# Performance work log

Hardware: AMD Instinct MI355X
Metric: run time of the kernel (lower is better)

## Reference

```python
import jax, jax.numpy as jnp
import numpy as np

EPS = 1e-5
V = 16  # num_nodes

def _bn(x, g, b, axes, ch):
    # training-mode BatchNorm (biased variance), channel axis = ch
    m = x.mean(axes, keepdims=True)
    v = x.var(axes, keepdims=True)
    sh = [1] * x.ndim
    sh[ch] = x.shape[ch]
    return (x - m) * jax.lax.rsqrt(v + EPS) * g.reshape(sh) + b.reshape(sh)

def _adp(nv1, nv2, max_num_neigh=1):
    # softmax(relu(nv1 @ nv2), dim=1), then keep entries > max(1/V, (k+1)-th largest) with straight-through mask
    A = jax.nn.softmax(jax.nn.relu(nv1 @ nv2), axis=1)
    kth = -jnp.sort(-A, axis=1)[:, max_num_neigh:max_num_neigh + 1]  # (k+1)-th largest per row == -kthvalue(-A, k+1)
    mask = ((A > 1.0 / A.shape[0]) & (A > kth)).astype(A.dtype)
    binm = jax.lax.stop_gradient(mask - A) + A  # straight-through estimator
    return A * binm

def _stgcn(x, A, gw, gb, b1g, b1b, tw, tb, b2g, b2b):
    # standard ST-GCN block with spatial kernel K=1, stride 1, identity residual (in==out)
    # x: (N,C,T,V)
    res = x
    y = jnp.einsum('oc,nctv->notv', gw, x) + gb[None, :, None, None]  # 1x1 conv
    y = jnp.einsum('nctv,vw->nctw', y, A)                              # graph aggregation
    y = jax.nn.relu(_bn(y, b1g, b1b, (0, 2, 3), 1))
    y = jax.lax.conv_general_dilated(y, tw[:, :, :, None], (1, 1), [(1, 1), (0, 0)],
                                     dimension_numbers=('NCHW', 'OIHW', 'NCHW'))  # temporal conv (kt,1)
    y = _bn(y + tb[None, :, None, None], b2g, b2b, (0, 2, 3), 1)
    return jax.nn.relu(y + res)

def _static(x, pw, pg, pb, tw, tg, tb):
    # x: (p,n,c,s)
    p, n, c, s = x.shape
    # p-branch: Conv1d(c->c, k=1, no bias) over node dim + BN1d (stats over n*s batch and length p)
    y = jnp.einsum('oc,pncs->nsop', pw, x)          # (n,s,c,p)
    y = _bn(y, pg, pb, (0, 1, 3), 2)
    # t-branch: grouped Conv1d over time, groups = p nodes, kernel 3, pad 1
    z = y.transpose(0, 3, 2, 1).reshape(n, p * c, s)
    z = jax.lax.conv_general_dilated(z, tw, (1,), [(1, 1)],
                                     dimension_numbers=('NCH', 'OIH', 'NCH'),
                                     feature_group_count=p)
    z = _bn(z, tg, tb, (0, 2), 1)
    return z.reshape(n, p, c, s).transpose(1, 0, 2, 3)  # (p,n,c,s)

def _forward(x, nv1, nv2,
             d1gw, d1gb, d1b1g, d1b1b, d1tw, d1tb, d1b2g, d1b2b,
             d2gw, d2gb, d2b1g, d2b1b, d2tw, d2tb, d2b2g, d2b2b,
             s1pw, s1pg, s1pb, s1tw, s1tg, s1tb,
             s2pw, s2pg, s2pb, s2tw, s2tg, s2tb):
    A = _adp(nv1, nv2, 1)
    d = _stgcn(x, A, d1gw, d1gb, d1b1g, d1b1b, d1tw, d1tb, d1b2g, d1b2b)
    d = _stgcn(d, A, d2gw, d2gb, d2b1g, d2b1b, d2tw, d2tb, d2b2g, d2b2b)
    d = d.max(axis=2)                      # (N,C,V) max over time
    xs = x.transpose(3, 0, 1, 2)           # (V,N,C,T)
    s = _static(xs, s1pw, s1pg, s1pb, s1tw, s1tg, s1tb)
    s = _static(s, s2pw, s2pg, s2pb, s2tw, s2tg, s2tb)
    s = s.transpose(1, 2, 3, 0).max(axis=2)  # (N,C,V)
    return jnp.concatenate([d, s], axis=2)   # (N,C,2V)

def setup_inputs():
    key = jax.random.key(0)
    N, C, T, kt = 32, 128, 256, 3
    ks = jax.random.split(key, 8)
    def nrm(k, sh, s=0.05):
        return jax.random.normal(k, sh, jnp.float32) * s
    inp = {'x': nrm(ks[0], (N, C, T, V), 1.0),
           'nv1': nrm(ks[1], (V, 64), 1.0),
           'nv2': nrm(ks[2], (64, V), 1.0)}
    def stgcn_p(k, pre):
        k1, k2 = jax.random.split(k)
        return {pre + 'gw': nrm(k1, (C, C)), pre + 'gb': jnp.zeros(C),
                pre + 'b1g': jnp.ones(C), pre + 'b1b': jnp.zeros(C),
                pre + 'tw': nrm(k2, (C, C, kt)), pre + 'tb': jnp.zeros(C),
                pre + 'b2g': jnp.ones(C), pre + 'b2b': jnp.zeros(C)}
    def static_p(k, pre):
        k1, k2 = jax.random.split(k)
        return {pre + 'pw': nrm(k1, (C, C)), pre + 'pg': jnp.ones(C), pre + 'pb': jnp.zeros(C),
                pre + 'tw': nrm(k2, (V * C, C, kt)), pre + 'tg': jnp.ones(V * C), pre + 'tb': jnp.zeros(V * C)}
    inp.update(stgcn_p(ks[3], 'd1'))
    inp.update(stgcn_p(ks[4], 'd2'))
    inp.update(static_p(ks[5], 's1'))
    inp.update(static_p(ks[6], 's2'))
    return inp

def reference(x, nv1, nv2,
              d1gw, d1gb, d1b1g, d1b1b, d1tw, d1tb, d1b2g, d1b2b,
              d2gw, d2gb, d2b1g, d2b1b, d2tw, d2tb, d2b2g, d2b2b,
              s1pw, s1pg, s1pb, s1tw, s1tg, s1tb,
              s2pw, s2pg, s2pb, s2tw, s2tg, s2tb):
    return _forward(x, nv1, nv2,
                    d1gw, d1gb, d1b1g, d1b1b, d1tw, d1tb, d1b2g, d1b2b,
                    d2gw, d2gb, d2b1g, d2b1b, d2tw, d2tb, d2b2g, d2b2b,
                    s1pw, s1pg, s1pb, s1tw, s1tg, s1tb,
                    s2pw, s2pg, s2pb, s2tw, s2tg, s2tb)
```

## Files before the change

### kernel.cpp

```cpp
#include <hip/hip_runtime.h>

#define EPSBN 1e-5f

typedef __attribute__((ext_vector_type(8))) __bf16 bf16x8;
typedef __attribute__((ext_vector_type(4))) float f32x4;
typedef __attribute__((ext_vector_type(8))) unsigned short us8;

__device__ inline unsigned short f2bf(float f) {
  __bf16 h = (__bf16)f;
  return __builtin_bit_cast(unsigned short, h);
}
__device__ inline float bf2f(unsigned short u) {
  __bf16 h = __builtin_bit_cast(__bf16, u);
  return (float)h;
}

__global__ void k_adj(const float* __restrict__ nv1, const float* __restrict__ nv2,
                      float* __restrict__ A, float* __restrict__ sA,
                      int* __restrict__ cntA, int* __restrict__ lvA, float* __restrict__ lvalA) {
  __shared__ float M[16][16];
  int tid = threadIdx.x;
  int i = tid >> 4, j = tid & 15;
  float acc = 0.f;
  #pragma unroll
  for (int k = 0; k < 64; ++k) acc += nv1[i*64+k] * nv2[k*16+j];
  M[i][j] = fmaxf(acc, 0.f);
  __syncthreads();
  if (tid < 16) {
    float m = -1e30f;
    for (int c = 0; c < 16; ++c) m = fmaxf(m, M[tid][c]);
    float e[16]; float s = 0.f;
    for (int c = 0; c < 16; ++c) { e[c] = expf(M[tid][c] - m); s += e[c]; }
    float inv = 1.f / s;
    float t1 = -1e30f, t2 = -1e30f;
    for (int c = 0; c < 16; ++c) {
      float a = e[c] * inv; e[c] = a;
      if (a > t1) { t2 = t1; t1 = a; }
      else if (a > t2) t2 = a;
    }
    for (int c = 0; c < 16; ++c) {
      bool keep = (e[c] > (1.0f/16.0f)) && (e[c] > t2);
      M[tid][c] = keep ? e[c] : 0.f;
    }
  }
  __syncthreads();
  A[tid] = M[tid>>4][tid&15];
  if (tid < 16) {
    float s = 0.f;
    int cnt = 0;
    for (int v = 0; v < 16; ++v) {
      float a = M[v][tid];
      s += a;
      if (a != 0.f) { lvA[tid*16 + cnt] = v; lvalA[tid*16 + cnt] = a; ++cnt; }
    }
    sA[tid] = s;
    cntA[tid] = cnt;
  }
}

__device__ inline void cvt_cw_seg(const float* w, unsigned short* o, int lidx) {
  o[lidx] = f2bf(w[lidx]);
}
__device__ inline void cvt_tw_seg(const float* w, unsigned short* o, int lidx) {
  int oo = lidx / 384;
  int r = lidx - oo*384;
  int tap = r >> 7, c = r & 127;
  o[lidx] = f2bf(w[(oo*128 + c)*3 + tap]);
}
__global__ __launch_bounds__(256) void k_cvt_dyn(
    const float* __restrict__ d1g, const float* __restrict__ d1t,
    const float* __restrict__ d2g, const float* __restrict__ d2t,
    unsigned short* __restrict__ O) {
  int b = blockIdx.x, tid = threadIdx.x;
  if (b < 64)        cvt_cw_seg(d1g, O,          b*256 + tid);
  else if (b < 256)  cvt_tw_seg(d1t, O + 16384, (b-64)*256 + tid);
  else if (b < 320)  cvt_cw_seg(d2g, O + 65536, (b-256)*256 + tid);
  else               cvt_tw_seg(d2t, O + 81920, (b-320)*256 + tid);
}
__global__ __launch_bounds__(256) void k_cvt_stat(
    const float* __restrict__ s1p, const float* __restrict__ s1t,
    const float* __restrict__ s2p, const float* __restrict__ s2t,
    unsigned short* __restrict__ S) {
  int b = blockIdx.x, tid = threadIdx.x;
  if (b < 64)        cvt_cw_seg(s1p, S,           b*256 + tid);
  else if (b < 3136) cvt_tw_seg(s1t, S + 16384,  (b-64)*256 + tid);
  else if (b < 3200) cvt_cw_seg(s2p, S + 802816, (b-3136)*256 + tid);
  else               cvt_tw_seg(s2t, S + 819200, (b-3200)*256 + tid);
}

__global__ __launch_bounds__(256) void k_xcvt(const float* __restrict__ x,
                                              unsigned short* __restrict__ xB,
                                              unsigned short* __restrict__ xS) {
  __shared__ float tl[64*128];
  int b = blockIdx.x; int n = b >> 6; int t0q = b & 63;
  int tid = threadIdx.x;
  const float* xb = x + (long)n*524288 + t0q*64;
  for (int idx = tid; idx < 2048; idx += 256) {
    int c = idx >> 4, q = idx & 15;
    float4 v = *(const float4*)(xb + (long)c*4096 + q*4);
    int cb = c >> 2, cl = c & 3;
    #pragma unroll
    for (int j = 0; j < 4; ++j)
      tl[(4*q+j)*128 + (((cb ^ q) & 31) << 2) + cl] = ((const float*)&v)[j];
  }
  __syncthreads();
  for (int idx = tid; idx < 1024; idx += 256) {
    int pos = idx >> 4, c8 = (idx & 15) << 3;
    int cb0 = c8 >> 2, cb1 = cb0 + 1, qp = pos >> 2;
    f32x4 v0 = *(const f32x4*)&tl[pos*128 + (((cb0 ^ qp) & 31) << 2)];
    f32x4 v1 = *(const f32x4*)&tl[pos*128 + (((cb1 ^ qp) & 31) << 2)];
    us8 pk;
    pk[0]=f2bf(v0.x); pk[1]=f2bf(v0.y); pk[2]=f2bf(v0.z); pk[3]=f2bf(v0.w);
    pk[4]=f2bf(v1.x); pk[5]=f2bf(v1.y); pk[6]=f2bf(v1.z); pk[7]=f2bf(v1.w);
    *(us8*)(xB + ((long)n*4096 + t0q*64 + pos)*128 + c8) = pk;
    int vv = pos & 15, tt = pos >> 4;
    *(us8*)(xS + ((long)(n*16+vv)*256 + t0q*4 + tt)*128 + c8) = pk;
  }
}

__global__ __launch_bounds__(256) void k_aggGconv(
    const unsigned short* __restrict__ xB,
    const int* __restrict__ cntA, const int* __restrict__ lvA, const float* __restrict__ lvalA,
    const unsigned short* __restrict__ Wb,
    unsigned short* __restrict__ out,
    const float* __restrict__ gb, const float* __restrict__ sAv,
    float* __restrict__ part)
{
  __shared__ __align__(16) unsigned short Th[64*128];
  __shared__ int cntS[16];
  __shared__ int lvS[256];
  __shared__ float lvalS[256];
  int b = blockIdx.x; int n = b >> 6; int off = (b & 63) << 6;
  int tid = threadIdx.x;
  if (tid < 16) cntS[tid] = cntA[tid];
  lvS[tid] = lvA[tid];
  lvalS[tid] = lvalA[tid];
  __syncthreads();
  const unsigned short* xbase = xB + ((long)n*4096 + off)*128;
  for (int idx = tid; idx < 1024; idx += 256) {
    int pos = idx >> 4, c8 = (idx & 15) << 3;
    int tt = pos >> 4, w = pos & 15;
    float s[8];
    #pragma unroll
    for (int k = 0; k < 8; ++k) s[k] = 0.f;
    int cw = cntS[w];
    for (int j = 0; j < cw; ++j) {
      int p = tt*16 + lvS[w*16 + j];
      float a = lvalS[w*16 + j];
      us8 raw = *(const us8*)(xbase + (long)p*128 + c8);
      #pragma unroll
      for (int k = 0; k < 8; ++k) s[k] += a * bf2f(raw[k]);
    }
    us8 pk;
    #pragma unroll
    for (int k = 0; k < 8; ++k) pk[k] = f2bf(s[k]);
    int byteoff = (pos << 8) + (c8 << 1);
    byteoff ^= ((pos & 7) << 4);
    *(us8*)((char*)Th + byteoff) = pk;
  }
  __syncthreads();
  int wv = tid >> 6, lane = tid & 63, l15 = lane & 15, lhi = lane >> 4;
  int o0 = wv << 5;
  f32x4 zz = {0.f,0.f,0.f,0.f};
  f32x4 acc[2][4];
  #pragma unroll
  for (int i = 0; i < 2; ++i)
    #pragma unroll
    for (int q = 0; q < 4; ++q) acc[i][q] = zz;
  const unsigned short* wr0 = Wb + (long)(o0 + l15)*128 + lhi*8;
  const unsigned short* wr1 = wr0 + 16*128;
  #pragma unroll
  for (int kk = 0; kk < 4; ++kk) {
    int kc = kk*32 + lhi*8;
    bf16x8 a0 = *(const bf16x8*)(wr0 + kk*32);
    bf16x8 a1 = *(const bf16x8*)(wr1 + kk*32);
    #pragma unroll
    for (int pf = 0; pf < 4; ++pf) {
      int row = pf*16 + l15;
      int byteoff = (row << 8) + (kc << 1);
      byteoff ^= ((row & 7) << 4);
      bf16x8 bh = *(const bf16x8*)((const char*)Th + byteoff);
      acc[0][pf] = __builtin_amdgcn_mfma_f32_16x16x32_bf16(a0, bh, acc[0][pf], 0, 0, 0);
      acc[1][pf] = __builtin_amdgcn_mfma_f32_16x16x32_bf16(a1, bh, acc[1][pf], 0, 0, 0);
    }
  }
  float s1a[2][4], s2a[2][4];
  #pragma unroll
  for (int i = 0; i < 2; ++i)
    #pragma unroll
    for (int j = 0; j < 4; ++j) { s1a[i][j] = 0.f; s2a[i][j] = 0.f; }
  unsigned short* og = out + ((long)n*4096 + off)*128;
  #pragma unroll
  for (int of = 0; of < 2; ++of) {
    int oc = o0 + of*16 + lhi*4;
    #pragma unroll
    for (int pf = 0; pf < 4; ++pf) {
      int pos = pf*16 + l15;
      f32x4 r = acc[of][pf];
      float s = sAv[l15];
      r.x += gb[oc+0]*s; r.y += gb[oc+1]*s;
      r.z += gb[oc+2]*s; r.w += gb[oc+3]*s;
      ushort4 pk;
      pk.x = f2bf(r.x); pk.y = f2bf(r.y); pk.z = f2bf(r.z); pk.w = f2bf(r.w);
      *(ushort4*)(og + (long)pos*128 + oc) = pk;
      #pragma unroll
      for (int j = 0; j < 4; ++j) { s1a[of][j] += r[j]; s2a[of][j] += r[j]*r[j]; }
    }
  }
  #pragma unroll
  for (int of = 0; of < 2; ++of)
    #pragma unroll
    for (int j = 0; j < 4; ++j) {
      float a = s1a[of][j], b2 = s2a[of][j];
      #pragma unroll
      for (int m = 1; m < 16; m <<= 1) { a += __shfl_xor(a, m); b2 += __shfl_xor(b2, m); }
      s1a[of][j] = a; s2a[of][j] = b2;
    }
  if (l15 == 0) {
    #pragma unroll
    for (int of = 0; of < 2; ++of) {
      int ch = o0 + of*16 + lhi*4;
      f32x4 w1 = {s1a[of][0], s1a[of][1], s1a[of][2], s1a[of][3]};
      f32x4 w2 = {s2a[of][0], s2a[of][1], s2a[of][2], s2a[of][3]};
      *(f32x4*)&part[(long)blockIdx.x*256 + ch] = w1;
      *(f32x4*)&part[(long)blockIdx.x*256 + 128 + ch] = w2;
    }
  }
}

__global__ __launch_bounds__(256) void k_combineAggGconv(
    const unsigned short* __restrict__ z, const unsigned short* __restrict__ xB,
    const int* __restrict__ cntA, const int* __restrict__ lvA, const float* __restrict__ lvalA,
    const float* __restrict__ sc, const float* __restrict__ sh,
    const unsigned short* __restrict__ Wb,
    unsigned short* __restrict__ r2, unsigned short* __restrict__ out,
    const float* __restrict__ gb, const float* __restrict__ sAv,
    float* __restrict__ part)
{
  __shared__ __align__(16) unsigned short rl[64*128];
  __shared__ __align__(16) unsigned short Th[64*128];
  __shared__ int cntS[16];
  __shared__ int lvS[256];
  __shared__ float lvalS[256];
  int b = blockIdx.x;
  int tid = threadIdx.x;
  if (tid < 16) cntS[tid] = cntA[tid];
  lvS[tid] = lvA[tid];
  lvalS[tid] = lvalA[tid];
  long zbase = (long)b * 8192;
  for (int idx = tid; idx < 1024; idx += 256) {
    int pos = idx >> 4, c8 = (idx & 15) << 3;
    us8 zr = *(const us8*)(z  + zbase + (long)pos*128 + c8);
    us8 xr = *(const us8*)(xB + zbase + (long)pos*128 + c8);
    us8 pr;
    #pragma unroll
    for (int k = 0; k < 8; ++k) {
      int cc = c8 + k;
      float v = bf2f(zr[k]) * sc[cc] + sh[cc] + bf2f(xr[k]);
      pr[k] = f2bf(fmaxf(v, 0.f));
    }
    *(us8*)(rl + pos*128 + c8) = pr;
    *(us8*)(r2 + zbase + (long)pos*128 + c8) = pr;
  }
  __syncthreads();
  for (int idx = tid; idx < 1024; idx += 256) {
    int pos = idx >> 4, c8 = (idx & 15) << 3;
    int tt = pos >> 4, w = pos & 15;
    float s[8];
    #pragma unroll
    for (int k = 0; k < 8; ++k) s[k] = 0.f;
    int cw = cntS[w];
    for (int j = 0; j < cw; ++j) {
      int p = tt*16 + lvS[w*16 + j];
      float a = lvalS[w*16 + j];
      us8 raw = *(const us8*)(rl + p*128 + c8);
      #pragma unroll
      for (int k = 0; k < 8; ++k) s[k] += a * bf2f(raw[k]);
    }
    us8 pk;
    #pragma unroll
    for (int k = 0; k < 8; ++k) pk[k] = f2bf(s[k]);
    int byteoff = (pos << 8) + (c8 << 1);
    byteoff ^= ((pos & 7) << 4);
    *(us8*)((char*)Th + byteoff) = pk;
  }
  __syncthreads();
  int wv = tid >> 6, lane = tid & 63, l15 = lane & 15, lhi = lane >> 4;
  int o0 = wv << 5;
  f32x4 zz = {0.f,0.f,0.f,0.f};
  f32x4 acc[2][4];
  #pragma unroll
  for (int i = 0; i < 2; ++i)
    #pragma unroll
    for (int q = 0; q < 4; ++q) acc[i][q] = zz;
  const unsigned short* wr0 = Wb + (long)(o0 + l15)*128 + lhi*8;
  const unsigned short* wr1 = wr0 + 16*128;
  #pragma unroll
  for (int kk = 0; kk < 4; ++kk) {
    int kc = kk*32 + lhi*8;
    bf16x8 a0 = *(const bf16x8*)(wr0 + kk*32);
    bf16x8 a1 = *(const bf16x8*)(wr1 + kk*32);
    #pragma unroll
    for (int pf = 0; pf < 4; ++pf) {
      int row = pf*16 + l15;
      int byteoff = (row << 8) + (kc << 1);
      byteoff ^= ((row & 7) << 4);
      bf16x8 bh = *(const bf16x8*)((const char*)Th + byteoff);
      acc[0][pf] = __builtin_amdgcn_mfma_f32_16x16x32_bf16(a0, bh, acc[0][pf], 0, 0, 0);
      acc[1][pf] = __builtin_amdgcn_mfma_f32_16x16x32_bf16(a1, bh, acc[1][pf], 0, 0, 0);
    }
  }
  float s1a[2][4], s2a[2][4];
  #pragma unroll
  for (int i = 0; i < 2; ++i)
    #pragma unroll
    for (int j = 0; j < 4; ++j) { s1a[i][j] = 0.f; s2a[i][j] = 0.f; }
  unsigned short* og = out + zbase;
  #pragma unroll
  for (int of = 0; of < 2; ++of) {
    int oc = o0 + of*16 + lhi*4;
    #pragma unroll
    for (int pf = 0; pf < 4; ++pf) {
      int pos = pf*16 + l15;
      f32x4 r = acc[of][pf];
      float s = sAv[l15];
      r.x += gb[oc+0]*s; r.y += gb[oc+1]*s;
      r.z += gb[oc+2]*s; r.w += gb[oc+3]*s;
      ushort4 pk;
      pk.x = f2bf(r.x); pk.y = f2bf(r.y); pk.z = f2bf(r.z); pk.w = f2bf(r.w);
      *(ushort4*)(og + (long)pos*128 + oc) = pk;
      #pragma unroll
      for (int j = 0; j < 4; ++j) { s1a[of][j] += r[j]; s2a[of][j] += r[j]*r[j]; }
    }
  }
  #pragma unroll
  for (int of = 0; of < 2; ++of)
    #pragma unroll
    for (int j = 0; j < 4; ++j) {
      float a = s1a[of][j], b2 = s2a[of][j];
      #pragma unroll
      for (int m = 1; m < 16; m <<= 1) { a += __shfl_xor(a, m); b2 += __shfl_xor(b2, m); }
      s1a[of][j] = a; s2a[of][j] = b2;
    }
  if (l15 == 0) {
    #pragma unroll
    for (int of = 0; of < 2; ++of) {
      int ch = o0 + of*16 + lhi*4;
      f32x4 w1 = {s1a[of][0], s1a[of][1], s1a[of][2], s1a[of][3]};
      f32x4 w2 = {s2a[of][0], s2a[of][1], s2a[of][2], s2a[of][3]};
      *(f32x4*)&part[(long)blockIdx.x*256 + ch] = w1;
      *(f32x4*)&part[(long)blockIdx.x*256 + 128 + ch] = w2;
    }
  }
}

template<int POSB, int HALO, int TAPS, int GROUPED_W, int IN_BN, int GROUPED_BN, int RELU_IN>
__global__ __launch_bounds__(256) void k_conv(
    const unsigned short* __restrict__ in, const unsigned short* __restrict__ Wb,
    unsigned short* __restrict__ out, int L,
    const float* __restrict__ isc, const float* __restrict__ ish,
    float* __restrict__ part)
{
  constexpr int TW = POSB + 2*HALO;
  constexpr int PF = POSB / 16;
  constexpr int KT = TAPS*128;
  __shared__ __align__(16) unsigned short Th[TW*128];
  int tid = threadIdx.x;
  int bpg = L / POSB;
  int g = blockIdx.x / bpg;
  int pos0 = (blockIdx.x - g*bpg) * POSB;
  const unsigned short* ing = in + (long)g*L*128;

  int cbase = (IN_BN && GROUPED_BN) ? ((g & 15) << 7) : 0;
  for (int idx = tid; idx < TW*16; idx += 256) {
    int row = idx >> 4;
    int c8 = (idx & 15) << 3;
    int gp = pos0 + row - HALO;
    us8 h = (us8)0;
    if (gp >= 0 && gp < L) {
      us8 raw = *(const us8*)(ing + (long)gp*128 + c8);
      if (IN_BN) {
        #pragma unroll
        for (int j = 0; j < 8; ++j) {
          int ci = cbase + c8 + j;
          float v = bf2f(raw[j]) * isc[ci] + ish[ci];
          if (RELU_IN) v = fmaxf(v, 0.f);
          h[j] = f2bf(v);
        }
      } else {
        h = raw;
      }
    }
    int byteoff = (row << 8) + (c8 << 1);
    byteoff ^= ((row & 7) << 4);
    *(us8*)((char*)Th + byteoff) = h;
  }
  __syncthreads();

  int wv = tid >> 6, lane = tid & 63, l15 = lane & 15, lhi = lane >> 4;
  int o0 = wv << 5;

  f32x4 zz = {0.f,0.f,0.f,0.f};
  f32x4 acc[2][PF];
  #pragma unroll
  for (int i = 0; i < 2; ++i)
    #pragma unroll
    for (int q = 0; q < PF; ++q) acc[i][q] = zz;

  const unsigned short* Wg = Wb + (GROUPED_W ? (long)(g & 15)*128*KT : 0);
  const unsigned short* wr0 = Wg + (long)(o0 + l15)*KT + lhi*8;
  const unsigned short* wr1 = wr0 + 16*KT;

  #pragma unroll
  for (int tap = 0; tap < TAPS; ++tap) {
    #pragma unroll
    for (int kk = 0; kk < 4; ++kk) {
      int kc = kk*32 + lhi*8;
      bf16x8 a0 = *(const bf16x8*)(wr0 + tap*128 + kk*32);
      bf16x8 a1 = *(const bf16x8*)(wr1 + tap*128 + kk*32);
      #pragma unroll
      for (int pf = 0; pf < PF; ++pf) {
        int row = pf*16 + l15 + tap*HALO;
        int byteoff = (row << 8) + (kc << 1);
        byteoff ^= ((row & 7) << 4);
        bf16x8 bh = *(const bf16x8*)((const char*)Th + byteoff);
        acc[0][pf] = __builtin_amdgcn_mfma_f32_16x16x32_bf16(a0, bh, acc[0][pf], 0, 0, 0);
        acc[1][pf] = __builtin_amdgcn_mfma_f32_16x16x32_bf16(a1, bh, acc[1][pf], 0, 0, 0);
      }
    }
  }

  float s1a[2][4], s2a[2][4];
  #pragma unroll
  for (int i = 0; i < 2; ++i)
    #pragma unroll
    for (int j = 0; j < 4; ++j) { s1a[i][j] = 0.f; s2a[i][j] = 0.f; }
  #pragma unroll
  for (int of = 0; of < 2; ++of)
    #pragma unroll
    for (int pf = 0; pf < PF; ++pf) {
      f32x4 r = acc[of][pf];
      #pragma unroll
      for (int j = 0; j < 4; ++j) { s1a[of][j] += r[j]; s2a[of][j] += r[j]*r[j]; }
    }
  #pragma unroll
  for (int of = 0; of < 2; ++of)
    #pragma unroll
    for (int j = 0; j < 4; ++j) {
      float a = s1a[of][j], b2 = s2a[of][j];
      #pragma unroll
      for (int m = 1; m < 16; m <<= 1) { a += __shfl_xor(a, m); b2 += __shfl_xor(b2, m); }
      s1a[of][j] = a; s2a[of][j] = b2;
    }
  if (l15 == 0) {
    #pragma unroll
    for (int of = 0; of < 2; ++of) {
      int ch = o0 + of*16 + lhi*4;
      f32x4 w1 = {s1a[of][0], s1a[of][1], s1a[of][2], s1a[of][3]};
      f32x4 w2 = {s2a[of][0], s2a[of][1], s2a[of][2], s2a[of][3]};
      *(f32x4*)&part[(long)blockIdx.x*256 + ch] = w1;
      *(f32x4*)&part[(long)blockIdx.x*256 + 128 + ch] = w2;
    }
  }

  __syncthreads();
  #pragma unroll
  for (int of = 0; of < 2; ++of) {
    int oc = o0 + of*16 + lhi*4;
    #pragma unroll
    for (int pf = 0; pf < PF; ++pf) {
      int pos = pf*16 + l15;
      f32x4 r = acc[of][pf];
      ushort4 pk;
      pk.x = f2bf(r.x); pk.y = f2bf(r.y); pk.z = f2bf(r.z); pk.w = f2bf(r.w);
      int byteoff = (pos << 8) + (oc << 1);
      byteoff ^= ((pos & 7) << 4);
      *(ushort4*)((char*)Th + byteoff) = pk;
    }
  }
  __syncthreads();
  unsigned short* og = out + ((long)g*L + pos0)*128;
  for (int idx = tid; idx < POSB*16; idx += 256) {
    int row = idx >> 4, c8 = (idx & 15) << 3;
    int byteoff = (row << 8) + (c8 << 1);
    byteoff ^= ((row & 7) << 4);
    us8 v = *(const us8*)((const char*)Th + byteoff);
    *(us8*)(og + (long)row*128 + c8) = v;
  }
}

__global__ __launch_bounds__(256) void k_bnfin128(const float* __restrict__ part,
                           const float* __restrict__ gamma, const float* __restrict__ beta,
                           float* __restrict__ sc, float* __restrict__ sh,
                           float invN, int nblk) {
  int c = blockIdx.x, tid = threadIdx.x;
  float s1 = 0.f, s2 = 0.f;
  for (int b = tid; b < nblk; b += 256) {
    s1 += part[b*256 + c];
    s2 += part[b*256 + 128 + c];
  }
  __shared__ float l1[256], l2[256];
  l1[tid] = s1; l2[tid] = s2;
  __syncthreads();
  for (int st = 128; st > 0; st >>= 1) {
    if (tid < st) { l1[tid] += l1[tid+st]; l2[tid] += l2[tid+st]; }
    __syncthreads();
  }
  if (tid == 0) {
    float mean = l1[0]*invN;
    float var  = l2[0]*invN - mean*mean;
    float s = gamma[c] * rsqrtf(var + EPSBN);
    sc[c] = s;
    sh[c] = beta[c] - mean*s;
  }
}

__global__ void k_bnfin2048(const float* __restrict__ part,
                            const float* __restrict__ gamma, const float* __restrict__ beta,
                            float* __restrict__ sc, float* __restrict__ sh, float invN) {
  int ch = blockIdx.x; int v = ch >> 7, c = ch & 127;
  int lane = threadIdx.x;
  int n = lane >> 1, bp = lane & 1;
  int blk = ((n*16 + v) << 1) + bp;
  float s1 = part[blk*256 + c];
  float s2 = part[blk*256 + 128 + c];
  for (int m = 32; m > 0; m >>= 1) { s1 += __shfl_down(s1, m); s2 += __shfl_down(s2, m); }
  if (lane == 0) {
    float mean = s1*invN;
    float var  = s2*invN - mean*mean;
    float s = gamma[ch] * rsqrtf(var + EPSBN);
    sc[ch] = s;
    sh[ch] = beta[ch] - mean*s;
  }
}

__global__ __launch_bounds__(256) void k_maxdyn(
    const unsigned short* __restrict__ z, const unsigned short* __restrict__ res,
    const float* __restrict__ sc, const float* __restrict__ sh,
    float* __restrict__ outp)
{
  int b = blockIdx.x; int n = b >> 4, v = b & 15;
  int tid = threadIdx.x; int c = tid & 127, h = tid >> 7;
  const unsigned short* zb = z   + ((long)n*4096 + v)*128 + c;
  const unsigned short* rb = res + ((long)n*4096 + v)*128 + c;
  float s = sc[c], bb = sh[c];
  float m = 0.f;
  for (int t = h; t < 256; t += 2) {
    float val = bf2f(zb[(long)t*2048]) * s + bb + bf2f(rb[(long)t*2048]);
    m = fmaxf(m, val);
  }
  __shared__ float red[256];
  red[tid] = m;
  __syncthreads();
  if (tid < 128)
    outp[(long)n*4096 + c*32 + v] = fmaxf(fmaxf(red[tid], red[tid+128]), 0.f);
}

__global__ __launch_bounds__(256) void k_maxstat(
    const unsigned short* __restrict__ z,
    const float* __restrict__ sc, const float* __restrict__ sh,
    float* __restrict__ outp)
{
  int b = blockIdx.x; int n = b >> 4, v = b & 15;
  int tid = threadIdx.x; int c = tid & 127, h = tid >> 7;
  const unsigned short* zb = z + (long)b*256*128 + c;
  float s = sc[v*128 + c], bb = sh[v*128 + c];
  float m = -1e30f;
  for (int t = h; t < 256; t += 2)
    m = fmaxf(m, bf2f(zb[t*128]) * s + bb);
  __shared__ float red[256];
  red[tid] = m;
  __syncthreads();
  if (tid < 128)
    outp[(long)n*4096 + c*32 + 16 + v] = fmaxf(red[tid], red[tid+128]);
}

extern "C" void kernel_launch(void* const* d_in, const int* in_sizes, int n_in,
                              void* d_out, int out_size, void* d_ws, size_t ws_size,
                              hipStream_t stream) {
  (void)in_sizes; (void)n_in; (void)out_size; (void)ws_size;
  const float* x     = (const float*)d_in[0];
  const float* nv1   = (const float*)d_in[1];
  const float* nv2   = (const float*)d_in[2];
  const float* d1gw  = (const float*)d_in[3];
  const float* d1gb  = (const float*)d_in[4];
  const float* d1b1g = (const float*)d_in[5];
  const float* d1b1b = (const float*)d_in[6];
  const float* d1tw  = (const float*)d_in[7];
  const float* d1b2g = (const float*)d_in[9];
  const float* d1b2b = (const float*)d_in[10];
  const float* d2gw  = (const float*)d_in[11];
  const float* d2gb  = (const float*)d_in[12];
  const float* d2b1g = (const float*)d_in[13];
  const float* d2b1b = (const float*)d_in[14];
  const float* d2tw  = (const float*)d_in[15];
  const float* d2b2g = (const float*)d_in[17];
  const float* d2b2b = (const float*)d_in[18];
  const float* s1pw  = (const float*)d_in[19];
  const float* s1pg  = (const float*)d_in[20];
  const float* s1pb  = (const float*)d_in[21];
  const float* s1tw  = (const float*)d_in[22];
  const float* s1tg  = (const float*)d_in[23];
  const float* s1tb  = (const float*)d_in[24];
  const float* s2pw  = (const float*)d_in[25];
  const float* s2pg  = (const float*)d_in[26];
  const float* s2pb  = (const float*)d_in[27];
  const float* s2tw  = (const float*)d_in[28];
  const float* s2tg  = (const float*)d_in[29];
  const float* s2tb  = (const float*)d_in[30];

  float* W = (float*)d_ws;
  float* Am  = W;
  float* sAv = W + 256;
  float* scA = W + 512;  float* shA = W + 640;
  float* scB = W + 768;  float* shB = W + 896;
  float* scC = W + 1024; float* shC = W + 1152;
  float* scD = W + 1280; float* shD = W + 1408;
  float* scE = W + 1536; float* shE = W + 1664;
  float* scG = W + 1792; float* shG = W + 1920;
  float* scF = W + 2048; float* shF = W + 4096;
  float* scH = W + 6144; float* shH = W + 8192;
  int*   cntA  = (int*)(W + 10240);
  int*   lvA   = (int*)(W + 10496);
  float* lvalA = W + 10752;
  float* A = W + 16384;
  float* B = A + 16777216;
  float* C = B + 16777216;
  float* part = C + 16777216;
  float* outp = (float*)d_out;

  unsigned short* A0 = (unsigned short*)A;
  unsigned short* A1 = (unsigned short*)(A + 8388608);
  unsigned short* B0 = (unsigned short*)B;
  unsigned short* B1 = (unsigned short*)(B + 8388608);
  unsigned short* C0 = (unsigned short*)C;
  unsigned short* C1 = (unsigned short*)(C + 8388608);

  unsigned short* OW = (unsigned short*)d_out;
  unsigned short* w_d1g = OW;
  unsigned short* w_d1t = OW + 16384;
  unsigned short* w_d2g = OW + 65536;
  unsigned short* w_d2t = OW + 81920;
  unsigned short* SW    = B1;
  unsigned short* w_s1p = SW;
  unsigned short* w_s1t = SW + 16384;
  unsigned short* w_s2p = SW + 802816;
  unsigned short* w_s2t = SW + 819200;

  k_adj<<<1, 256, 0, stream>>>(nv1, nv2, Am, sAv, cntA, lvA, lvalA);
  k_cvt_dyn<<<512, 256, 0, stream>>>(d1gw, d1tw, d2gw, d2tw, OW);
  k_xcvt<<<2048, 256, 0, stream>>>(x, A0, A1);

  k_aggGconv<<<2048, 256, 0, stream>>>(A0, cntA, lvA, lvalA, w_d1g, B0, d1gb, sAv, part);
  k_bnfin128<<<128, 256, 0, stream>>>(part, d1b1g, d1b1b, scA, shA, 1.f/131072.f, 2048);
  k_conv<128,16,3,0,1,0,1><<<1024, 256, 0, stream>>>(B0, w_d1t, C0, 4096, scA, shA, part);
  k_bnfin128<<<128, 256, 0, stream>>>(part, d1b2g, d1b2b, scB, shB, 1.f/131072.f, 1024);
  k_combineAggGconv<<<2048, 256, 0, stream>>>(C0, A0, cntA, lvA, lvalA, scB, shB, w_d2g,
                                              B0, C1, d2gb, sAv, part);
  k_bnfin128<<<128, 256, 0, stream>>>(part, d2b1g, d2b1b, scC, shC, 1.f/131072.f, 2048);
  k_conv<128,16,3,0,1,0,1><<<1024, 256, 0, stream>>>(C1, w_d2t, B1, 4096, scC, shC, part);
  k_bnfin128<<<128, 256, 0, stream>>>(part, d2b2g, d2b2b, scD, shD, 1.f/131072.f, 1024);
  k_maxdyn<<<512, 256, 0, stream>>>(B1, B0, scD, shD, outp);

  k_cvt_stat<<<6272, 256, 0, stream>>>(s1pw, s1tw, s2pw, s2tw, SW);
  k_conv<128,0,1,0,0,0,0><<<1024, 256, 0, stream>>>(A1, w_s1p, C0, 256, nullptr, nullptr, part);
  k_bnfin128<<<128, 256, 0, stream>>>(part, s1pg, s1pb, scE, shE, 1.f/131072.f, 1024);
  k_conv<128,1,3,1,1,0,0><<<1024, 256, 0, stream>>>(C0, w_s1t, A0, 256, scE, shE, part);
  k_bnfin2048<<<2048, 64, 0, stream>>>(part, s1tg, s1tb, scF, shF, 1.f/8192.f);
  k_conv<128,0,1,0,1,1,0><<<1024, 256, 0, stream>>>(A0, w_s2p, C0, 256, scF, shF, part);
  k_bnfin128<<<128, 256, 0, stream>>>(part, s2pg, s2pb, scG, shG, 1.f/131072.f, 1024);
  k_conv<128,1,3,1,1,0,0><<<1024, 256, 0, stream>>>(C0, w_s2t, A0, 256, scG, shG, part);
  k_bnfin2048<<<2048, 64, 0, stream>>>(part, s2tg, s2tb, scH, shH, 1.f/8192.f);
  k_maxstat<<<512, 256, 0, stream>>>(A0, scH, shH, outp);
}
```

Baseline: 354.3 us.

## Fuse BN stat finalization into producer kernels via atomics and last-block reduction

New measurement: 1.174 ms. 231% more time.

```diff
diff --git a/kernel.cpp b/kernel.cpp
--- a/kernel.cpp
+++ b/kernel.cpp
@@ -15,11 +15,67 @@
   return (float)h;
 }
 
-__global__ void k_adj(const float* __restrict__ nv1, const float* __restrict__ nv2,
-                      float* __restrict__ A, float* __restrict__ sA,
-                      int* __restrict__ cntA, int* __restrict__ lvA, float* __restrict__ lvalA) {
+__device__ inline void bn_finalize_tail(float* acc, int* cnt, int nblk, int NCH,
+    const float* __restrict__ gamma, const float* __restrict__ beta,
+    float* __restrict__ sc, float* __restrict__ sh, float invN, int tid) {
+  __syncthreads();
+  __shared__ int lastFlag;
+  if (tid == 0) {
+    __threadfence();
+    lastFlag = (atomicAdd(cnt, 1) == nblk - 1) ? 1 : 0;
+  }
+  __syncthreads();
+  if (lastFlag) {
+    __threadfence();
+    for (int ch = tid; ch < NCH; ch += 256) {
+      float s1 = __hip_atomic_load(acc + ch,        __ATOMIC_RELAXED, __HIP_MEMORY_SCOPE_AGENT);
+      float s2 = __hip_atomic_load(acc + NCH + ch,  __ATOMIC_RELAXED, __HIP_MEMORY_SCOPE_AGENT);
+      float mean = s1 * invN;
+      float var  = s2 * invN - mean * mean;
+      float s = gamma[ch] * rsqrtf(var + EPSBN);
+      sc[ch] = s;
+      sh[ch] = beta[ch] - mean * s;
+    }
+  }
+}
+
+__device__ inline void cvt_cw_seg(const float* w, unsigned short* o, int lidx) {
+  o[lidx] = f2bf(w[lidx]);
+}
+__device__ inline void cvt_tw_seg(const float* w, unsigned short* o, int lidx) {
+  int oo = lidx / 384;
+  int r = lidx - oo*384;
+  int tap = r >> 7, c = r & 127;
+  o[lidx] = f2bf(w[(oo*128 + c)*3 + tap]);
+}
+__global__ __launch_bounds__(256) void k_setup(
+    const float* __restrict__ nv1, const float* __restrict__ nv2,
+    float* __restrict__ A, float* __restrict__ sA,
+    int* __restrict__ cntA, int* __restrict__ lvA, float* __restrict__ lvalA,
+    const float* __restrict__ d1g, const float* __restrict__ d1t,
+    const float* __restrict__ d2g, const float* __restrict__ d2t,
+    unsigned short* __restrict__ O,
+    const float* __restrict__ s1p, const float* __restrict__ s1t,
+    const float* __restrict__ s2p, const float* __restrict__ s2t,
+    unsigned short* __restrict__ S)
+{
+  int b = blockIdx.x, tid = threadIdx.x;
+  if (b < 512) {
+    if (b < 64)        cvt_cw_seg(d1g, O,          b*256 + tid);
+    else if (b < 256)  cvt_tw_seg(d1t, O + 16384, (b-64)*256 + tid);
+    else if (b < 320)  cvt_cw_seg(d2g, O + 65536, (b-256)*256 + tid);
+    else               cvt_tw_seg(d2t, O + 81920, (b-320)*256 + tid);
+    return;
+  }
+  if (b < 6784) {
+    int sb = b - 512;
+    if (sb < 64)        cvt_cw_seg(s1p, S,           sb*256 + tid);
+    else if (sb < 3136) cvt_tw_seg(s1t, S + 16384,  (sb-64)*256 + tid);
+    else if (sb < 3200) cvt_cw_seg(s2p, S + 802816, (sb-3136)*256 + tid);
+    else                cvt_tw_seg(s2t, S + 819200, (sb-3200)*256 + tid);
+    return;
+  }
   __shared__ float M[16][16];
-  int tid = threadIdx.x;
   int i = tid >> 4, j = tid & 15;
   float acc = 0.f;
   #pragma unroll
@@ -58,36 +114,6 @@
   }
 }
 
-__device__ inline void cvt_cw_seg(const float* w, unsigned short* o, int lidx) {
-  o[lidx] = f2bf(w[lidx]);
-}
-__device__ inline void cvt_tw_seg(const float* w, unsigned short* o, int lidx) {
-  int oo = lidx / 384;
-  int r = lidx - oo*384;
-  int tap = r >> 7, c = r & 127;
-  o[lidx] = f2bf(w[(oo*128 + c)*3 + tap]);
-}
-__global__ __launch_bounds__(256) void k_cvt_dyn(
-    const float* __restrict__ d1g, const float* __restrict__ d1t,
-    const float* __restrict__ d2g, const float* __restrict__ d2t,
-    unsigned short* __restrict__ O) {
-  int b = blockIdx.x, tid = threadIdx.x;
-  if (b < 64)        cvt_cw_seg(d1g, O,          b*256 + tid);
-  else if (b < 256)  cvt_tw_seg(d1t, O + 16384, (b-64)*256 + tid);
-  else if (b < 320)  cvt_cw_seg(d2g, O + 65536, (b-256)*256 + tid);
-  else               cvt_tw_seg(d2t, O + 81920, (b-320)*256 + tid);
-}
-__global__ __launch_bounds__(256) void k_cvt_stat(
-    const float* __restrict__ s1p, const float* __restrict__ s1t,
-    const float* __restrict__ s2p, const float* __restrict__ s2t,
-    unsigned short* __restrict__ S) {
-  int b = blockIdx.x, tid = threadIdx.x;
-  if (b < 64)        cvt_cw_seg(s1p, S,           b*256 + tid);
-  else if (b < 3136) cvt_tw_seg(s1t, S + 16384,  (b-64)*256 + tid);
-  else if (b < 3200) cvt_cw_seg(s2p, S + 802816, (b-3136)*256 + tid);
-  else               cvt_tw_seg(s2t, S + 819200, (b-3200)*256 + tid);
-}
-
 __global__ __launch_bounds__(256) void k_xcvt(const float* __restrict__ x,
                                               unsigned short* __restrict__ xB,
                                               unsigned short* __restrict__ xS) {
@@ -124,7 +150,9 @@
     const unsigned short* __restrict__ Wb,
     unsigned short* __restrict__ out,
     const float* __restrict__ gb, const float* __restrict__ sAv,
-    float* __restrict__ part)
+    float* __restrict__ acc_g, int* __restrict__ cnt_g,
+    const float* __restrict__ gamma, const float* __restrict__ beta,
+    float* __restrict__ scO, float* __restrict__ shO, float invN)
 {
   __shared__ __align__(16) unsigned short Th[64*128];
   __shared__ int cntS[16];
@@ -218,14 +246,15 @@
     }
   if (l15 == 0) {
     #pragma unroll
-    for (int of = 0; of < 2; ++of) {
-      int ch = o0 + of*16 + lhi*4;
-      f32x4 w1 = {s1a[of][0], s1a[of][1], s1a[of][2], s1a[of][3]};
-      f32x4 w2 = {s2a[of][0], s2a[of][1], s2a[of][2], s2a[of][3]};
-      *(f32x4*)&part[(long)blockIdx.x*256 + ch] = w1;
-      *(f32x4*)&part[(long)blockIdx.x*256 + 128 + ch] = w2;
-    }
-  }
+    for (int of = 0; of < 2; ++of)
+      #pragma unroll
+      for (int j = 0; j < 4; ++j) {
+        int ch = o0 + of*16 + lhi*4 + j;
+        atomicAdd(acc_g + ch, s1a[of][j]);
+        atomicAdd(acc_g + 128 + ch, s2a[of][j]);
+      }
+  }
+  bn_finalize_tail(acc_g, cnt_g, gridDim.x, 128, gamma, beta, scO, shO, invN, tid);
 }
 
 __global__ __launch_bounds__(256) void k_combineAggGconv(
@@ -235,7 +264,9 @@
     const unsigned short* __restrict__ Wb,
     unsigned short* __restrict__ r2, unsigned short* __restrict__ out,
     const float* __restrict__ gb, const float* __restrict__ sAv,
-    float* __restrict__ part)
+    float* __restrict__ acc_g, int* __restrict__ cnt_g,
+    const float* __restrict__ gamma, const float* __restrict__ beta,
+    float* __restrict__ scO, float* __restrict__ shO, float invN)
 {
   __shared__ __align__(16) unsigned short rl[64*128];
   __shared__ __align__(16) unsigned short Th[64*128];
@@ -344,26 +375,30 @@
     }
   if (l15 == 0) {
     #pragma unroll
-    for (int of = 0; of < 2; ++of) {
-      int ch = o0 + of*16 + lhi*4;
-      f32x4 w1 = {s1a[of][0], s1a[of][1], s1a[of][2], s1a[of][3]};
-      f32x4 w2 = {s2a[of][0], s2a[of][1], s2a[of][2], s2a[of][3]};
-      *(f32x4*)&part[(long)blockIdx.x*256 + ch] = w1;
-      *(f32x4*)&part[(long)blockIdx.x*256 + 128 + ch] = w2;
-    }
-  }
-}
-
-template<int POSB, int HALO, int TAPS, int GROUPED_W, int IN_BN, int GROUPED_BN, int RELU_IN>
+    for (int of = 0; of < 2; ++of)
+      #pragma unroll
+      for (int j = 0; j < 4; ++j) {
+        int ch = o0 + of*16 + lhi*4 + j;
+        atomicAdd(acc_g + ch, s1a[of][j]);
+        atomicAdd(acc_g + 128 + ch, s2a[of][j]);
+      }
+  }
+  bn_finalize_tail(acc_g, cnt_g, gridDim.x, 128, gamma, beta, scO, shO, invN, tid);
+}
+
+template<int POSB, int HALO, int TAPS, int GROUPED_W, int IN_BN, int GROUPED_BN, int RELU_IN, int BNMODE>
 __global__ __launch_bounds__(256) void k_conv(
     const unsigned short* __restrict__ in, const unsigned short* __restrict__ Wb,
     unsigned short* __restrict__ out, int L,
     const float* __restrict__ isc, const float* __restrict__ ish,
-    float* __restrict__ part)
+    float* __restrict__ acc_g, int* __restrict__ cnt_g,
+    const float* __restrict__ gamma, const float* __restrict__ beta,
+    float* __restrict__ scO, float* __restrict__ shO, float invN)
 {
   constexpr int TW = POSB + 2*HALO;
   constexpr int PF = POSB / 16;
   constexpr int KT = TAPS*128;
+  constexpr int NCH = (BNMODE == 2) ? 2048 : 128;
   __shared__ __align__(16) unsigned short Th[TW*128];
   int tid = threadIdx.x;
   int bpg = L / POSB;
@@ -452,15 +487,16 @@
       for (int m = 1; m < 16; m <<= 1) { a += __shfl_xor(a, m); b2 += __shfl_xor(b2, m); }
       s1a[of][j] = a; s2a[of][j] = b2;
     }
+  int chbase = (BNMODE == 2) ? ((g & 15) << 7) : 0;
   if (l15 == 0) {
     #pragma unroll
-    for (int of = 0; of < 2; ++of) {
-      int ch = o0 + of*16 + lhi*4;
-      f32x4 w1 = {s1a[of][0], s1a[of][1], s1a[of][2], s1a[of][3]};
-      f32x4 w2 = {s2a[of][0], s2a[of][1], s2a[of][2], s2a[of][3]};
-      *(f32x4*)&part[(long)blockIdx.x*256 + ch] = w1;
-      *(f32x4*)&part[(long)blockIdx.x*256 + 128 + ch] = w2;
-    }
+    for (int of = 0; of < 2; ++of)
+      #pragma unroll
+      for (int j = 0; j < 4; ++j) {
+        int ch = chbase + o0 + of*16 + lhi*4 + j;
+        atomicAdd(acc_g + ch, s1a[of][j]);
+        atomicAdd(acc_g + NCH + ch, s2a[of][j]);
+      }
   }
 
   __syncthreads();
@@ -487,51 +523,8 @@
     us8 v = *(const us8*)((const char*)Th + byteoff);
     *(us8*)(og + (long)row*128 + c8) = v;
   }
-}
-
-__global__ __launch_bounds__(256) void k_bnfin128(const float* __restrict__ part,
-                           const float* __restrict__ gamma, const float* __restrict__ beta,
-                           float* __restrict__ sc, float* __restrict__ sh,
-                           float invN, int nblk) {
-  int c = blockIdx.x, tid = threadIdx.x;
-  float s1 = 0.f, s2 = 0.f;
-  for (int b = tid; b < nblk; b += 256) {
-    s1 += part[b*256 + c];
-    s2 += part[b*256 + 128 + c];
-  }
-  __shared__ float l1[256], l2[256];
-  l1[tid] = s1; l2[tid] = s2;
-  __syncthreads();
-  for (int st = 128; st > 0; st >>= 1) {
-    if (tid < st) { l1[tid] += l1[tid+st]; l2[tid] += l2[tid+st]; }
-    __syncthreads();
-  }
-  if (tid == 0) {
-    float mean = l1[0]*invN;
-    float var  = l2[0]*invN - mean*mean;
-    float s = gamma[c] * rsqrtf(var + EPSBN);
-    sc[c] = s;
-    sh[c] = beta[c] - mean*s;
-  }
-}
-
-__global__ void k_bnfin2048(const float* __restrict__ part,
-                            const float* __restrict__ gamma, const float* __restrict__ beta,
-                            float* __restrict__ sc, float* __restrict__ sh, float invN) {
-  int ch = blockIdx.x; int v = ch >> 7, c = ch & 127;
-  int lane = threadIdx.x;
-  int n = lane >> 1, bp = lane & 1;
-  int blk = ((n*16 + v) << 1) + bp;
-  float s1 = part[blk*256 + c];
-  float s2 = part[blk*256 + 128 + c];
-  for (int m = 32; m > 0; m >>= 1) { s1 += __shfl_down(s1, m); s2 += __shfl_down(s2, m); }
-  if (lane == 0) {
-    float mean = s1*invN;
-    float var  = s2*invN - mean*mean;
-    float s = gamma[ch] * rsqrtf(var + EPSBN);
-    sc[ch] = s;
-    sh[ch] = beta[ch] - mean*s;
-  }
+
+  bn_finalize_tail(acc_g, cnt_g, gridDim.x, NCH, gamma, beta, scO, shO, invN, tid);
 }
 
 __global__ __launch_bounds__(256) void k_maxdyn(
@@ -623,10 +616,18 @@
   int*   cntA  = (int*)(W + 10240);
   int*   lvA   = (int*)(W + 10496);
   float* lvalA = W + 10752;
-  float* A = W + 16384;
+  float* accZ1  = W + 11264;
+  float* accZ2  = W + 11520;
+  float* accZ3  = W + 11776;
+  float* accZ4  = W + 12032;
+  float* accS1P = W + 12288;
+  float* accS2P = W + 12544;
+  float* accS1T = W + 12800;
+  float* accS2T = W + 16896;
+  int*   cnts   = (int*)(W + 20992);
+  float* A = W + 24576;
   float* B = A + 16777216;
   float* C = B + 16777216;
-  float* part = C + 16777216;
   float* outp = (float*)d_out;
 
   unsigned short* A0 = (unsigned short*)A;
@@ -647,29 +648,33 @@
   unsigned short* w_s2p = SW + 802816;
   unsigned short* w_s2t = SW + 819200;
 
-  k_adj<<<1, 256, 0, stream>>>(nv1, nv2, Am, sAv, cntA, lvA, lvalA);
-  k_cvt_dyn<<<512, 256, 0, stream>>>(d1gw, d1tw, d2gw, d2tw, OW);
+  const float iN  = 1.f/131072.f;
+  const float iNg = 1.f/8192.f;
+
+  hipMemsetAsync(W + 11264, 0, (20992 - 11264 + 8) * 4, stream);
+  k_setup<<<6785, 256, 0, stream>>>(nv1, nv2, Am, sAv, cntA, lvA, lvalA,
+                                    d1gw, d1tw, d2gw, d2tw, OW,
+                                    s1pw, s1tw, s2pw, s2tw, SW);
   k_xcvt<<<2048, 256, 0, stream>>>(x, A0, A1);
 
-  k_aggGconv<<<2048, 256, 0, stream>>>(A0, cntA, lvA, lvalA, w_d1g, B0, d1gb, sAv, part);
-  k_bnfin128<<<128, 256, 0, stream>>>(part, d1b1g, d1b1b, scA, shA, 1.f/131072.f, 2048);
-  k_conv<128,16,3,0,1,0,1><<<1024, 256, 0, stream>>>(B0, w_d1t, C0, 4096, scA, shA, part);
-  k_bnfin128<<<128, 256, 0, stream>>>(part, d1b2g, d1b2b, scB, shB, 1.f/131072.f, 1024);
+  k_aggGconv<<<2048, 256, 0, stream>>>(A0, cntA, lvA, lvalA, w_d1g, B0, d1gb, sAv,
+                                       accZ1, cnts+0, d1b1g, d1b1b, scA, shA, iN);
+  k_conv<128,16,3,0,1,0,1,1><<<1024, 256, 0, stream>>>(B0, w_d1t, C0, 4096, scA, shA,
+                                       accZ2, cnts+1, d1b2g, d1b2b, scB, shB, iN);
   k_combineAggGconv<<<2048, 256, 0, stream>>>(C0, A0, cntA, lvA, lvalA, scB, shB, w_d2g,
-                                              B0, C1, d2gb, sAv, part);
-  k_bnfin128<<<128, 256, 0, stream>>>(part, d2b1g, d2b1b, scC, shC, 1.f/131072.f, 2048);
-  k_conv<128,16,3,0,1,0,1><<<1024, 256, 0, stream>>>(C1, w_d2t, B1, 4096, scC, shC, part);
-  k_bnfin128<<<128, 256, 0, stream>>>(part, d2b2g, d2b2b, scD, shD, 1.f/131072.f, 1024);
-  k_maxdyn<<<512, 256, 0, stream>>>(B1, B0, scD, shD, outp);
-
-  k_cvt_stat<<<6272, 256, 0, stream>>>(s1pw, s1tw, s2pw, s2tw, SW);
-  k_conv<128,0,1,0,0,0,0><<<1024, 256, 0, stream>>>(A1, w_s1p, C0, 256, nullptr, nullptr, part);
-  k_bnfin128<<<128, 256, 0, stream>>>(part, s1pg, s1pb, scE, shE, 1.f/131072.f, 1024);
-  k_conv<128,1,3,1,1,0,0><<<1024, 256, 0, stream>>>(C0, w_s1t, A0, 256, scE, shE, part);
-  k_bnfin2048<<<2048, 64, 0, stream>>>(part, s1tg, s1tb, scF, shF, 1.f/8192.f);
-  k_conv<128,0,1,0,1,1,0><<<1024, 256, 0, stream>>>(A0, w_s2p, C0, 256, scF, shF, part);
-  k_bnfin128<<<128, 256, 0, stream>>>(part, s2pg, s2pb, scG, shG, 1.f/131072.f, 1024);
-  k_conv<128,1,3,1,1,0,0><<<1024, 256, 0, stream>>>(C0, w_s2t, A0, 256, scG, shG, part);
-  k_bnfin2048<<<2048, 64, 0, stream>>>(part, s2tg, s2tb, scH, shH, 1.f/8192.f);
-  k_maxstat<<<512, 256, 0, stream>>>(A0, scH, shH, outp);
-}
+                                       B0, C1, d2gb, sAv,
+                                       accZ3, cnts+2, d2b1g, d2b1b, scC, shC, iN);
+  k_conv<128,16,3,0,1,0,1,1><<<1024, 256, 0, stream>>>(C1, w_d2t, A0, 4096, scC, shC,
+                                       accZ4, cnts+3, d2b2g, d2b2b, scD, shD, iN);
+  k_maxdyn<<<512, 256, 0, stream>>>(A0, B0, scD, shD, outp);
+
+  k_conv<128,0,1,0,0,0,0,1><<<1024, 256, 0, stream>>>(A1, w_s1p, C0, 256, nullptr, nullptr,
+                                       accS1P, cnts+4, s1pg, s1pb, scE, shE, iN);
+  k_conv<128,1,3,1,1,0,0,2><<<1024, 256, 0, stream>>>(C0, w_s1t, A1, 256, scE, shE,
+                                       accS1T, cnts+5, s1tg, s1tb, scF, shF, iNg);
+  k_conv<128,0,1,0,1,1,0,1><<<1024, 256, 0, stream>>>(A1, w_s2p, C0, 256, scF, shF,
+                                       accS2P, cnts+6, s2pg, s2pb, scG, shG, iN);
+  k_conv<128,1,3,1,1,0,0,2><<<1024, 256, 0, stream>>>(C0, w_s2t, A1, 256, scG, shG,
+                                       accS2T, cnts+7, s2tg, s2tb, scH, shH, iNg);
+  k_maxstat<<<512, 256, 0, stream>>>(A1, scH, shH, outp);
+}
```
